# Kernel optimization log

Measured on AMD Instinct MI355X. Metric: run time of the kernel, lower is better.

The kernel has to match this reference:

```python
import jax, jax.numpy as jnp
import numpy as np

N_HEADS = 4
TAU = 0.1

def _ln(x, w, b):
    m = jnp.mean(x, axis=-1, keepdims=True)
    v = jnp.mean(jnp.square(x - m), axis=-1, keepdims=True)
    return (x - m) / jnp.sqrt(v + 1e-6) * w + b

def _l2norm(x):
    # torch F.normalize(dim=1): x / max(||x||_2, 1e-12)
    n = jnp.linalg.norm(x, axis=1, keepdims=True)
    return x / jnp.maximum(n, 1e-12)

def _sincos_pe(T, dim):
    pos = jnp.arange(T, dtype=jnp.float32)[:, None]
    div = jnp.exp(jnp.arange(0, dim, 2, dtype=jnp.float32) * (-np.log(10000.0) / dim))
    ang = pos * div[None, :]
    # interleave: even indices sin, odd indices cos
    return jnp.stack([jnp.sin(ang), jnp.cos(ang)], axis=-1).reshape(T, dim)

def reference(x, p1_w, p1_b, pln1_w, pln1_b, p2_w, pln2_w, pln2_b,
              in_proj_w, in_proj_b, out_proj_w, out_proj_b,
              ln1_w, ln1_b, lin1_w, lin1_b, lin2_w, lin2_b, ln2_w, ln2_b, head_w):
    B, T, D = x.shape
    E = p2_w.shape[0]           # bottleneck_dim = 256
    H = N_HEADS
    hd = E // H
    # projector: Linear -> LN -> GELU -> Linear(no bias) -> LN
    h = jax.nn.gelu(_ln(x.reshape(B * T, D) @ p1_w.T + p1_b, pln1_w, pln1_b), approximate=False)
    h = _ln(h @ p2_w.T, pln2_w, pln2_b).reshape(B, T, E)
    h = h + _sincos_pe(T, E)[None]
    causal = jnp.tril(jnp.ones((T, T), dtype=bool))
    L = in_proj_w.shape[0]
    for i in range(L):  # post-norm TransformerEncoderLayer
        qkv = h @ in_proj_w[i].T + in_proj_b[i]        # [B,T,3E]
        q, k, v = jnp.split(qkv, 3, axis=-1)
        q = q.reshape(B, T, H, hd).transpose(0, 2, 1, 3)
        k = k.reshape(B, T, H, hd).transpose(0, 2, 1, 3)
        v = v.reshape(B, T, H, hd).transpose(0, 2, 1, 3)
        scores = jnp.einsum('bhtd,bhsd->bhts', q, k) / np.float32(np.sqrt(hd))
        scores = jnp.where(causal[None, None], scores, -jnp.inf)
        probs = jax.nn.softmax(scores, axis=-1)        # materialized attn probs (eager path)
        attn = jnp.einsum('bhts,bhsd->bhtd', probs, v).transpose(0, 2, 1, 3).reshape(B, T, E)
        attn = attn @ out_proj_w[i].T + out_proj_b[i]
        h = _ln(h + attn, ln1_w[i], ln1_b[i])
        ff = jax.nn.gelu(h @ lin1_w[i].T + lin1_b[i], approximate=False) @ lin2_w[i].T + lin2_b[i]
        h = _ln(h + ff, ln2_w[i], ln2_b[i])
    flat = _l2norm(h.reshape(B * T, E))
    wn = _l2norm(head_w)
    return (flat @ wn.T / TAU).reshape(B, T, -1)

def setup_inputs() -> dict:
    key = jax.random.key(0)
    ks = jax.random.split(key, 8)
    B, T, D, E, HID, CLS, L = 2048, 20, 2048, 256, 1024, 1000, 2
    s = 0.02
    def w(k, shape):
        return jax.random.normal(k, shape, jnp.float32) * s
    return {
        'x': jax.random.normal(ks[0], (B, T, D), jnp.float32),
        'p1_w': w(ks[1], (HID, D)), 'p1_b': jnp.zeros((HID,), jnp.float32),
        'pln1_w': jnp.ones((HID,), jnp.float32), 'pln1_b': jnp.zeros((HID,), jnp.float32),
        'p2_w': w(ks[2], (E, HID)),
        'pln2_w': jnp.ones((E,), jnp.float32), 'pln2_b': jnp.zeros((E,), jnp.float32),
        'in_proj_w': w(ks[3], (L, 3 * E, E)), 'in_proj_b': jnp.zeros((L, 3 * E), jnp.float32),
        'out_proj_w': w(ks[4], (L, E, E)), 'out_proj_b': jnp.zeros((L, E), jnp.float32),
        'ln1_w': jnp.ones((L, E), jnp.float32), 'ln1_b': jnp.zeros((L, E), jnp.float32),
        'lin1_w': w(ks[5], (L, 4 * E, E)), 'lin1_b': jnp.zeros((L, 4 * E), jnp.float32),
        'lin2_w': w(ks[6], (L, E, 4 * E)), 'lin2_b': jnp.zeros((L, E), jnp.float32),
        'ln2_w': jnp.ones((L, E), jnp.float32), 'ln2_b': jnp.zeros((L, E), jnp.float32),
        'head_w': w(ks[7], (CLS, E)),
    }
```

## Files before the change

kernel.cpp:

```cpp
#include <hip/hip_runtime.h>
#include <math.h>

#define CDIV(a,b) (((a)+(b)-1)/(b))

typedef unsigned short bfu;
typedef short   s16x8 __attribute__((ext_vector_type(8)));
typedef float   f32x4 __attribute__((ext_vector_type(4)));

#define GLOAD16(gp, lp) __builtin_amdgcn_global_load_lds( \
    (const __attribute__((address_space(1))) void*)(gp),  \
    (__attribute__((address_space(3))) void*)(lp), 16, 0, 0)

static __device__ __forceinline__ float gelu_exact(float x) {
    return 0.5f * x * (1.0f + erff(x * 0.7071067811865475f));
}
static __device__ __forceinline__ bfu f2bf(float x) {
    unsigned int u = __float_as_uint(x);
    unsigned int r = u + 0x7fffu + ((u >> 16) & 1u);
    return (bfu)(r >> 16);
}
static __device__ __forceinline__ float bf2f(bfu b) {
    return __uint_as_float(((unsigned int)b) << 16);
}
static __device__ __forceinline__ float wave_sum(float v) {
    #pragma unroll
    for (int off = 32; off; off >>= 1) v += __shfl_xor(v, off, 64);
    return v;
}

__global__ __launch_bounds__(256)
void cvt_kernel(const float* __restrict__ in, bfu* __restrict__ out, int n4)
{
    int i = blockIdx.x * 256 + threadIdx.x;
    const int stride = gridDim.x * 256;
    for (; i < n4; i += stride) {
        float4 f = ((const float4*)in)[i];
        ushort4 o;
        o.x = f2bf(f.x); o.y = f2bf(f.y); o.z = f2bf(f.z); o.w = f2bf(f.w);
        ((ushort4*)out)[i] = o;
    }
}

__global__ __launch_bounds__(256)
void cvt6_kernel(const float* __restrict__ s0, const float* __restrict__ s1,
                 const float* __restrict__ s2, const float* __restrict__ s3,
                 const float* __restrict__ s4, const float* __restrict__ s5,
                 bfu* __restrict__ dst)
{
    const int c0 = 524288;
    const int c1 = c0 + 65536;
    const int c2 = c1 + 98304;
    const int c3 = c2 + 32768;
    const int c4 = c3 + 131072;
    const int c5 = c4 + 131072;
    int i = blockIdx.x * 256 + threadIdx.x;
    const int stride = gridDim.x * 256;
    for (; i < c5; i += stride) {
        const float* s; int base;
        if      (i < c0) { s = s0; base = 0;  }
        else if (i < c1) { s = s1; base = c0; }
        else if (i < c2) { s = s2; base = c1; }
        else if (i < c3) { s = s3; base = c2; }
        else if (i < c4) { s = s4; base = c3; }
        else             { s = s5; base = c4; }
        float4 f = ((const float4*)s)[i - base];
        ushort4 o;
        o.x = f2bf(f.x); o.y = f2bf(f.y); o.z = f2bf(f.z); o.w = f2bf(f.w);
        ((ushort4*)dst)[i] = o;
    }
}

__global__ __launch_bounds__(256)
void pe_kernel(float* __restrict__ pe)
{
    const int t = blockIdx.x;
    const int c = threadIdx.x;
    const float div = expf((float)(c & ~1) * (-9.210340371976184f / 256.0f));
    const float ang = (float)t * div;
    pe[t * 256 + c] = (c & 1) ? cosf(ang) : sinf(ang);
}

template<bool GELU_EP, bool OUT_BF16>
__global__ __launch_bounds__(512, 2)
void mfma_gemm256(const bfu* __restrict__ A, const bfu* __restrict__ W,
                  const float* __restrict__ bias, void* __restrict__ Cv,
                  int M, int N, int K, float scale, int ntx)
{
    __shared__ bfu lds[2][2][8192];

    const int tid  = threadIdx.x;
    const int lane = tid & 63;
    const int wv   = tid >> 6;
    const int nwg  = gridDim.x;
    const int lid  = (nwg & 7) ? (int)blockIdx.x
                               : ((int)blockIdx.x & 7) * (nwg >> 3) + ((int)blockIdx.x >> 3);
    const int row0 = (lid / ntx) * 256;
    const int col0 = (lid % ntx) * 256;

    const int srow = wv * 16 + (lane >> 2);
    const int sk   = ((lane & 3) ^ ((lane >> 2) & 3)) * 8;
    const bfu* aS0 = A + (size_t)(row0 + srow)       * K + sk;
    const bfu* aS1 = A + (size_t)(row0 + srow + 128) * K + sk;
    const bfu* wS0 = W + (size_t)(col0 + srow)       * K + sk;
    const bfu* wS1 = W + (size_t)(col0 + srow + 128) * K + sk;
    const int dOff = wv * 512;

    const int wr = wv >> 2, wc = wv & 3;
    const int fr = lane & 15;
    const int slot = (((lane >> 4) ^ (fr & 3))) * 8;

    f32x4 acc[8][4];
    #pragma unroll
    for (int i = 0; i < 8; ++i)
        #pragma unroll
        for (int j = 0; j < 4; ++j) acc[i][j] = (f32x4)0.f;

    const int nt = K >> 5;

#define STAGE256(b_, t_) do { \
    const size_t ko_ = (size_t)(t_) * 32; \
    GLOAD16(aS0 + ko_, &lds[b_][0][dOff]); \
    GLOAD16(aS1 + ko_, &lds[b_][0][4096 + dOff]); \
    GLOAD16(wS0 + ko_, &lds[b_][1][dOff]); \
    GLOAD16(wS1 + ko_, &lds[b_][1][4096 + dOff]); \
} while (0)

    STAGE256(0, 0);
    STAGE256(1, 1);

    int cur = 0;
    for (int t = 0; t < nt; ++t) {
        if (t + 1 < nt) asm volatile("s_waitcnt vmcnt(4)" ::: "memory");
        else            asm volatile("s_waitcnt vmcnt(0)" ::: "memory");
        asm volatile("s_barrier" ::: "memory");

        const bfu* Ab = lds[cur][0];
        const bfu* Wb = lds[cur][1];

        s16x8 bfr[4], afr[8];
        #pragma unroll
        for (int j = 0; j < 4; ++j)
            bfr[j] = *(const s16x8*)&Wb[(wc * 64 + j * 16 + fr) * 32 + slot];
        #pragma unroll
        for (int i = 0; i < 4; ++i)
            afr[i] = *(const s16x8*)&Ab[(wr * 128 + i * 16 + fr) * 32 + slot];

        __builtin_amdgcn_s_setprio(1);
        #pragma unroll
        for (int i = 0; i < 4; ++i)
            #pragma unroll
            for (int j = 0; j < 4; ++j)
                acc[i][j] = __builtin_amdgcn_mfma_f32_16x16x32_bf16(afr[i], bfr[j], acc[i][j], 0, 0, 0);
        __builtin_amdgcn_s_setprio(0);

        #pragma unroll
        for (int i = 4; i < 8; ++i)
            afr[i] = *(const s16x8*)&Ab[(wr * 128 + i * 16 + fr) * 32 + slot];

        __builtin_amdgcn_s_setprio(1);
        #pragma unroll
        for (int i = 4; i < 8; ++i)
            #pragma unroll
            for (int j = 0; j < 4; ++j)
                acc[i][j] = __builtin_amdgcn_mfma_f32_16x16x32_bf16(afr[i], bfr[j], acc[i][j], 0, 0, 0);
        __builtin_amdgcn_s_setprio(0);

        asm volatile("s_barrier" ::: "memory");
        if (t + 2 < nt) STAGE256(cur, t + 2);
        cur ^= 1;
    }
#undef STAGE256

    #pragma unroll
    for (int i = 0; i < 8; ++i) {
        const int r = row0 + wr * 128 + 16 * i + (lane >> 4) * 4;
        #pragma unroll
        for (int j = 0; j < 4; ++j) {
            const int c = col0 + wc * 64 + 16 * j + fr;
            if (c < N) {
                const float bsum = bias ? bias[c] : 0.f;
                #pragma unroll
                for (int rr = 0; rr < 4; ++rr) {
                    float v = acc[i][j][rr] + bsum;
                    if (GELU_EP) v = gelu_exact(v);
                    v *= scale;
                    if (OUT_BF16) ((bfu*)Cv)[(size_t)(r + rr) * N + c] = f2bf(v);
                    else          ((float*)Cv)[(size_t)(r + rr) * N + c] = v;
                }
            }
        }
    }
}

template<bool RES, bool ADD_PE>
__global__ __launch_bounds__(512, 2)
void mfma_gemm_ln(const bfu* __restrict__ A, const bfu* __restrict__ W,
                  const float* __restrict__ bias, const float* __restrict__ R,
                  const float* __restrict__ lnw, const float* __restrict__ lnb,
                  const float* __restrict__ pe, float* __restrict__ Yf,
                  bfu* __restrict__ Yb, int M, int K, int T)
{
    __shared__ bfu ldsA[2][4096];
    __shared__ bfu ldsW[2][8192];

    const int tid  = threadIdx.x;
    const int lane = tid & 63;
    const int wv   = tid >> 6;
    const int nwg  = gridDim.x;
    const int lid  = (nwg & 7) ? (int)blockIdx.x
                               : ((int)blockIdx.x & 7) * (nwg >> 3) + ((int)blockIdx.x >> 3);
    const int row0 = lid * 128;

    const int srow = wv * 16 + (lane >> 2);
    const int sk   = ((lane & 3) ^ ((lane >> 2) & 3)) * 8;
    const bfu* aS  = A + (size_t)(row0 + srow) * K + sk;
    const bfu* wS0 = W + (size_t)(srow)        * K + sk;
    const bfu* wS1 = W + (size_t)(srow + 128)  * K + sk;
    const int dOff = wv * 512;

    const int wr = wv >> 2, wc = wv & 3;
    const int fr = lane & 15;
    const int g4 = lane >> 4;
    const int slot = ((g4 ^ (fr & 3))) * 8;

    f32x4 acc[4][4];
    #pragma unroll
    for (int i = 0; i < 4; ++i)
        #pragma unroll
        for (int j = 0; j < 4; ++j) acc[i][j] = (f32x4)0.f;

    const int nt = K >> 5;

#define STAGELN(b_, t_) do { \
    const size_t ko_ = (size_t)(t_) * 32; \
    GLOAD16(aS  + ko_, &ldsA[b_][dOff]); \
    GLOAD16(wS0 + ko_, &ldsW[b_][dOff]); \
    GLOAD16(wS1 + ko_, &ldsW[b_][4096 + dOff]); \
} while (0)

    STAGELN(0, 0);
    STAGELN(1, 1);

    int cur = 0;
    for (int t = 0; t < nt; ++t) {
        if (t + 1 < nt) asm volatile("s_waitcnt vmcnt(3)" ::: "memory");
        else            asm volatile("s_waitcnt vmcnt(0)" ::: "memory");
        asm volatile("s_barrier" ::: "memory");

        const bfu* Ab = ldsA[cur];
        const bfu* Wb = ldsW[cur];

        s16x8 bfr[4], afr[4];
        #pragma unroll
        for (int j = 0; j < 4; ++j)
            bfr[j] = *(const s16x8*)&Wb[(wc * 64 + j * 16 + fr) * 32 + slot];
        #pragma unroll
        for (int i = 0; i < 4; ++i)
            afr[i] = *(const s16x8*)&Ab[(wr * 64 + i * 16 + fr) * 32 + slot];

        __builtin_amdgcn_s_setprio(1);
        #pragma unroll
        for (int i = 0; i < 4; ++i)
            #pragma unroll
            for (int j = 0; j < 4; ++j)
                acc[i][j] = __builtin_amdgcn_mfma_f32_16x16x32_bf16(afr[i], bfr[j], acc[i][j], 0, 0, 0);
        __builtin_amdgcn_s_setprio(0);

        asm volatile("s_barrier" ::: "memory");
        if (t + 2 < nt) STAGELN(cur, t + 2);
        cur ^= 1;
    }
#undef STAGELN

    float* red   = (float*)ldsA;
    float* stats = red + 1024;

    float bj[4];
    #pragma unroll
    for (int j = 0; j < 4; ++j)
        bj[j] = bias ? bias[wc * 64 + j * 16 + fr] : 0.f;

    #pragma unroll
    for (int i = 0; i < 4; ++i) {
        #pragma unroll
        for (int rr = 0; rr < 4; ++rr) {
            const int rl = wr * 64 + i * 16 + g4 * 4 + rr;
            const size_t r = (size_t)(row0 + rl);
            float s = 0.f, q = 0.f;
            #pragma unroll
            for (int j = 0; j < 4; ++j) {
                float v = acc[i][j][rr] + bj[j];
                if (RES) v += R[r * 256 + (wc * 64 + j * 16 + fr)];
                acc[i][j][rr] = v;
                s += v; q += v * v;
            }
            #pragma unroll
            for (int off = 1; off < 16; off <<= 1) {
                s += __shfl_xor(s, off, 64);
                q += __shfl_xor(q, off, 64);
            }
            if (fr == 0) { red[rl * 4 + wc] = s; red[512 + rl * 4 + wc] = q; }
        }
    }
    __syncthreads();
    if (tid < 128) {
        const float s = red[tid*4+0] + red[tid*4+1] + red[tid*4+2] + red[tid*4+3];
        const float q = red[512+tid*4+0] + red[512+tid*4+1] + red[512+tid*4+2] + red[512+tid*4+3];
        const float mean = s * (1.f / 256.f);
        const float var  = q * (1.f / 256.f) - mean * mean;
        stats[tid]       = mean;
        stats[128 + tid] = rsqrtf(var + 1e-6f);
    }
    __syncthreads();

    float lw[4], lb[4];
    #pragma unroll
    for (int j = 0; j < 4; ++j) {
        const int c = wc * 64 + j * 16 + fr;
        lw[j] = lnw[c]; lb[j] = lnb[c];
    }
    #pragma unroll
    for (int i = 0; i < 4; ++i) {
        #pragma unroll
        for (int rr = 0; rr < 4; ++rr) {
            const int rl = wr * 64 + i * 16 + g4 * 4 + rr;
            const size_t r = (size_t)(row0 + rl);
            const float mean = stats[rl], rstd = stats[128 + rl];
            const int tmod = (int)(r % (size_t)T);
            #pragma unroll
            for (int j = 0; j < 4; ++j) {
                const int c = wc * 64 + j * 16 + fr;
                float y = (acc[i][j][rr] - mean) * rstd * lw[j] + lb[j];
                if (ADD_PE) y += pe[tmod * 256 + c];
                Yf[r * 256 + c] = y;
                Yb[r * 256 + c] = f2bf(y);
            }
        }
    }
}

__global__ __launch_bounds__(256)
void ln1024_kernel(const bfu* __restrict__ X, const float* __restrict__ w,
                   const float* __restrict__ b, bfu* __restrict__ Y)
{
    __shared__ float sbuf[4];
    const int row = blockIdx.x;
    const bfu* xr = X + (size_t)row * 1024;

    ushort4 t4 = *(const ushort4*)(xr + threadIdx.x * 4);
    float v[4] = {bf2f(t4.x), bf2f(t4.y), bf2f(t4.z), bf2f(t4.w)};

    float s = v[0] + v[1] + v[2] + v[3];
    s = wave_sum(s);
    const int lane = threadIdx.x & 63, wid = threadIdx.x >> 6;
    if (lane == 0) sbuf[wid] = s;
    __syncthreads();
    const float mean = (sbuf[0] + sbuf[1] + sbuf[2] + sbuf[3]) * (1.f / 1024.f);

    float q = 0.f;
    #pragma unroll
    for (int j = 0; j < 4; ++j) { float d = v[j] - mean; q += d * d; }
    q = wave_sum(q);
    __syncthreads();
    if (lane == 0) sbuf[wid] = q;
    __syncthreads();
    const float var  = (sbuf[0] + sbuf[1] + sbuf[2] + sbuf[3]) * (1.f / 1024.f);
    const float rstd = rsqrtf(var + 1e-6f);

    ushort4 o;
    #pragma unroll
    for (int j = 0; j < 4; ++j) {
        const int c = threadIdx.x * 4 + j;
        float y = gelu_exact((v[j] - mean) * rstd * w[c] + b[c]);
        ((bfu*)&o)[j] = f2bf(y);
    }
    *(ushort4*)(Y + (size_t)row * 1024 + threadIdx.x * 4) = o;
}

__global__ __launch_bounds__(64)
void attn_kernel(const bfu* __restrict__ qkv, bfu* __restrict__ out,
                 int B, int T, int H)
{
    __shared__ float qs[20][65];
    __shared__ float ks[20][65];
    __shared__ float vs[20][65];
    __shared__ float probs[64];

    const int blk = blockIdx.x;
    const int b = blk / H;
    const int h = blk % H;
    const int tid = threadIdx.x;

    for (int t = 0; t < T; ++t) {
        const bfu* base = qkv + (size_t)(b * T + t) * 768 + h * 64 + tid;
        qs[t][tid] = bf2f(base[0]);
        ks[t][tid] = bf2f(base[256]);
        vs[t][tid] = bf2f(base[512]);
    }
    __syncthreads();

    for (int t = 0; t < T; ++t) {
        float sc = -INFINITY;
        if (tid <= t) {
            float s = 0.f;
            #pragma unroll
            for (int d = 0; d < 64; ++d) s = fmaf(qs[t][d], ks[tid][d], s);
            sc = s * 0.125f;
        }
        float m = sc;
        #pragma unroll
        for (int off = 32; off; off >>= 1) m = fmaxf(m, __shfl_xor(m, off, 64));
        float p = (tid <= t) ? expf(sc - m) : 0.f;
        float sum = p;
        #pragma unroll
        for (int off = 32; off; off >>= 1) sum += __shfl_xor(sum, off, 64);
        p /= sum;
        probs[tid] = p;
        __syncthreads();

        float o = 0.f;
        for (int s = 0; s <= t; ++s) o = fmaf(probs[s], vs[s][tid], o);
        out[(size_t)(b * T + t) * 256 + h * 64 + tid] = f2bf(o);
        __syncthreads();
    }
}

__global__ __launch_bounds__(256)
void l2norm_kernel(const float* __restrict__ X, bfu* __restrict__ Y)
{
    const int row  = blockIdx.x * 4 + (threadIdx.x >> 6);
    const int lane = threadIdx.x & 63;
    float4 v = *(const float4*)(X + (size_t)row * 256 + lane * 4);
    float n = sqrtf(wave_sum(v.x*v.x + v.y*v.y + v.z*v.z + v.w*v.w));
    n = 1.f / fmaxf(n, 1e-12f);
    ushort4 o = {f2bf(v.x*n), f2bf(v.y*n), f2bf(v.z*n), f2bf(v.w*n)};
    *(ushort4*)(Y + (size_t)row * 256 + lane * 4) = o;
}

extern "C" void kernel_launch(void* const* d_in, const int* in_sizes, int n_in,
                              void* d_out, int out_size, void* d_ws, size_t ws_size,
                              hipStream_t stream)
{
    const float* x         = (const float*)d_in[0];
    const float* p1_w      = (const float*)d_in[1];
    const float* p1_b      = (const float*)d_in[2];
    const float* pln1_w    = (const float*)d_in[3];
    const float* pln1_b    = (const float*)d_in[4];
    const float* p2_w      = (const float*)d_in[5];
    const float* pln2_w    = (const float*)d_in[6];
    const float* pln2_b    = (const float*)d_in[7];
    const float* in_proj_w = (const float*)d_in[8];
    const float* in_proj_b = (const float*)d_in[9];
    const float* out_proj_w= (const float*)d_in[10];
    const float* out_proj_b= (const float*)d_in[11];
    const float* ln1_w     = (const float*)d_in[12];
    const float* ln1_b     = (const float*)d_in[13];
    const float* lin1_w    = (const float*)d_in[14];
    const float* lin1_b    = (const float*)d_in[15];
    const float* lin2_w    = (const float*)d_in[16];
    const float* lin2_b    = (const float*)d_in[17];
    const float* ln2_w     = (const float*)d_in[18];
    const float* ln2_b     = (const float*)d_in[19];
    const float* head_w    = (const float*)d_in[20];

    const int B = 2048, T = 20, E = 256, HID = 1024, CLS = 1000, L = 2, H = 4;
    const int M = B * T;
    const int D = 2048;

    char* p = (char*)d_ws;
    bfu*   xb     = (bfu*)p;    p += (size_t)M * D * 2;
    bfu*   h1b    = (bfu*)p;    p += (size_t)M * HID * 2;
    bfu*   wblk   = (bfu*)p;    p += (size_t)3932160 * 2;
    bfu*   wnb    = (bfu*)p;    p += (size_t)1024 * E * 2;
    float* pe     = (float*)p;  p += (size_t)T * 256 * 4;

    char* q = (char*)xb;
    float* h      = (float*)q;  q += (size_t)M * E * 4;
    bfu*   hb     = (bfu*)q;    q += (size_t)M * E * 2;
    bfu*   abf    = (bfu*)q;    q += (size_t)M * E * 2;

    bfu* p1wb  = wblk;
    bfu* p2wb  = p1wb  + (size_t)HID * D;
    bfu* qkvwb = p2wb  + (size_t)E * HID;
    bfu* outwb = qkvwb + (size_t)L * 3 * E * E;
    bfu* l1wb  = outwb + (size_t)L * E * E;
    bfu* l2wb  = l1wb  + (size_t)L * 4 * E * E;

    float* out   = (float*)d_out;
    bfu*   qkvb  = (bfu*)d_out;

    cvt_kernel<<<2048, 256, 0, stream>>>(x, xb, M * D / 4);
    cvt6_kernel<<<2048, 256, 0, stream>>>(p1_w, p2_w, in_proj_w, out_proj_w, lin1_w, lin2_w, wblk);
    pe_kernel<<<T, 256, 0, stream>>>(pe);

    mfma_gemm256<false, true><<<dim3((M/256) * (HID/256)), 512, 0, stream>>>(
        xb, p1wb, p1_b, h1b, M, HID, D, 1.f, HID/256);
    ln1024_kernel<<<M, 256, 0, stream>>>(h1b, pln1_w, pln1_b, h1b);
    mfma_gemm_ln<false, true><<<dim3(M/128), 512, 0, stream>>>(
        h1b, p2wb, nullptr, nullptr, pln2_w, pln2_b, pe, h, hb, M, HID, T);

    for (int l = 0; l < L; ++l) {
        mfma_gemm256<false, true><<<dim3(3 * (M/256)), 512, 0, stream>>>(
            hb, qkvwb + (size_t)l * 3*E*E, in_proj_b + (size_t)l * 3*E, qkvb, M, 3*E, E, 1.f, 3);
        attn_kernel<<<B * H, 64, 0, stream>>>(qkvb, abf, B, T, H);
        mfma_gemm_ln<true, false><<<dim3(M/128), 512, 0, stream>>>(
            abf, outwb + (size_t)l * E*E, out_proj_b + (size_t)l * E, h,
            ln1_w + (size_t)l * E, ln1_b + (size_t)l * E, nullptr, h, hb, M, E, T);
        mfma_gemm256<true, true><<<dim3(4 * (M/256)), 512, 0, stream>>>(
            hb, l1wb + (size_t)l * 4*E*E, lin1_b + (size_t)l * 4*E, h1b, M, HID, E, 1.f, 4);
        mfma_gemm_ln<true, false><<<dim3(M/128), 512, 0, stream>>>(
            h1b, l2wb + (size_t)l * E*4*E, lin2_b + (size_t)l * E, h,
            ln2_w + (size_t)l * E, ln2_b + (size_t)l * E, nullptr, h, hb, M, HID, T);
    }

    l2norm_kernel<<<M/4, 256, 0, stream>>>(h, hb);
    l2norm_kernel<<<CLS/4, 256, 0, stream>>>(head_w, wnb);
    mfma_gemm256<false, false><<<dim3(4 * (M/256)), 512, 0, stream>>>(
        hb, wnb, nullptr, out, M, CLS, E, 10.f, 4);
}
```

Measured before the change: 1.234 ms.

## Fuse final L2 normalization into last GEMM+LN, refine LDS swizzle, vectorize attention loads

The last layer's FFN-output GEMM+LayerNorm kernel now also computes each row's L2 norm with a cross-wave reduction in shared memory. It writes the normalized bf16 rows directly, which removes the separate l2norm kernel launch and the fp32 write and re-read of h. The LDS swizzle in both MFMA GEMM kernels adds an extra XOR term to cut bank conflicts on fragment reads. The attention kernel loads Q, K and V with 8-byte vector loads instead of scalar 2-byte loads. The new swizzle must stay consistent between the staging writes and the fragment reads, or results will be wrong.

```diff
diff --git a/kernel.cpp b/kernel.cpp
--- a/kernel.cpp
+++ b/kernel.cpp
@@ -98,7 +98,7 @@
     const int col0 = (lid % ntx) * 256;
 
     const int srow = wv * 16 + (lane >> 2);
-    const int sk   = ((lane & 3) ^ ((lane >> 2) & 3)) * 8;
+    const int sk   = ((lane & 3) ^ ((lane >> 2) & 3) ^ (lane >> 4)) * 8;
     const bfu* aS0 = A + (size_t)(row0 + srow)       * K + sk;
     const bfu* aS1 = A + (size_t)(row0 + srow + 128) * K + sk;
     const bfu* wS0 = W + (size_t)(col0 + srow)       * K + sk;
@@ -107,7 +107,7 @@
 
     const int wr = wv >> 2, wc = wv & 3;
     const int fr = lane & 15;
-    const int slot = (((lane >> 4) ^ (fr & 3))) * 8;
+    const int slot = (((lane >> 4) ^ (fr & 3) ^ ((fr >> 2) & 3))) * 8;
 
     f32x4 acc[8][4];
     #pragma unroll
@@ -192,7 +192,7 @@
     }
 }
 
-template<bool RES, bool ADD_PE>
+template<bool RES, bool ADD_PE, bool L2N>
 __global__ __launch_bounds__(512, 2)
 void mfma_gemm_ln(const bfu* __restrict__ A, const bfu* __restrict__ W,
                   const float* __restrict__ bias, const float* __restrict__ R,
@@ -212,7 +212,7 @@
     const int row0 = lid * 128;
 
     const int srow = wv * 16 + (lane >> 2);
-    const int sk   = ((lane & 3) ^ ((lane >> 2) & 3)) * 8;
+    const int sk   = ((lane & 3) ^ ((lane >> 2) & 3) ^ (lane >> 4)) * 8;
     const bfu* aS  = A + (size_t)(row0 + srow) * K + sk;
     const bfu* wS0 = W + (size_t)(srow)        * K + sk;
     const bfu* wS1 = W + (size_t)(srow + 128)  * K + sk;
@@ -221,7 +221,7 @@
     const int wr = wv >> 2, wc = wv & 3;
     const int fr = lane & 15;
     const int g4 = lane >> 4;
-    const int slot = ((g4 ^ (fr & 3))) * 8;
+    const int slot = ((g4 ^ (fr & 3) ^ ((fr >> 2) & 3))) * 8;
 
     f32x4 acc[4][4];
     #pragma unroll
@@ -327,13 +327,46 @@
             const size_t r = (size_t)(row0 + rl);
             const float mean = stats[rl], rstd = stats[128 + rl];
             const int tmod = (int)(r % (size_t)T);
+            float ysq = 0.f;
             #pragma unroll
             for (int j = 0; j < 4; ++j) {
                 const int c = wc * 64 + j * 16 + fr;
                 float y = (acc[i][j][rr] - mean) * rstd * lw[j] + lb[j];
                 if (ADD_PE) y += pe[tmod * 256 + c];
-                Yf[r * 256 + c] = y;
-                Yb[r * 256 + c] = f2bf(y);
+                if (!L2N) {
+                    Yf[r * 256 + c] = y;
+                    Yb[r * 256 + c] = f2bf(y);
+                } else {
+                    acc[i][j][rr] = y;
+                    ysq += y * y;
+                }
+            }
+            if (L2N) {
+                #pragma unroll
+                for (int off = 1; off < 16; off <<= 1) ysq += __shfl_xor(ysq, off, 64);
+                if (fr == 0) red[rl * 4 + wc] = ysq;
+            }
+        }
+    }
+    if (L2N) {
+        __syncthreads();
+        if (tid < 128) {
+            const float n = sqrtf(red[tid*4+0] + red[tid*4+1] + red[tid*4+2] + red[tid*4+3]);
+            stats[tid] = 1.f / fmaxf(n, 1e-12f);
+        }
+        __syncthreads();
+        #pragma unroll
+        for (int i = 0; i < 4; ++i) {
+            #pragma unroll
+            for (int rr = 0; rr < 4; ++rr) {
+                const int rl = wr * 64 + i * 16 + g4 * 4 + rr;
+                const size_t r = (size_t)(row0 + rl);
+                const float rn = stats[rl];
+                #pragma unroll
+                for (int j = 0; j < 4; ++j) {
+                    const int c = wc * 64 + j * 16 + fr;
+                    Yb[r * 256 + c] = f2bf(acc[i][j][rr] * rn);
+                }
             }
         }
     }
@@ -391,11 +424,19 @@
     const int h = blk % H;
     const int tid = threadIdx.x;
 
-    for (int t = 0; t < T; ++t) {
-        const bfu* base = qkv + (size_t)(b * T + t) * 768 + h * 64 + tid;
-        qs[t][tid] = bf2f(base[0]);
-        ks[t][tid] = bf2f(base[256]);
-        vs[t][tid] = bf2f(base[512]);
+    const bfu* base0 = qkv + (size_t)(b * T) * 768 + h * 64;
+    #pragma unroll
+    for (int m = 0; m < 3; ++m) {
+        const bfu* src = base0 + m * 256;
+        float (*dst)[65] = (m == 0) ? qs : (m == 1) ? ks : vs;
+        #pragma unroll
+        for (int i = 0; i < 5; ++i) {
+            const int idx = i * 64 + tid;
+            const int t = idx >> 4, s = (idx & 15) * 4;
+            ushort4 u = *(const ushort4*)(src + (size_t)t * 768 + s);
+            dst[t][s+0] = bf2f(u.x); dst[t][s+1] = bf2f(u.y);
+            dst[t][s+2] = bf2f(u.z); dst[t][s+3] = bf2f(u.w);
+        }
     }
     __syncthreads();
 
@@ -496,24 +537,29 @@
     mfma_gemm256<false, true><<<dim3((M/256) * (HID/256)), 512, 0, stream>>>(
         xb, p1wb, p1_b, h1b, M, HID, D, 1.f, HID/256);
     ln1024_kernel<<<M, 256, 0, stream>>>(h1b, pln1_w, pln1_b, h1b);
-    mfma_gemm_ln<false, true><<<dim3(M/128), 512, 0, stream>>>(
+    mfma_gemm_ln<false, true, false><<<dim3(M/128), 512, 0, stream>>>(
         h1b, p2wb, nullptr, nullptr, pln2_w, pln2_b, pe, h, hb, M, HID, T);
 
     for (int l = 0; l < L; ++l) {
         mfma_gemm256<false, true><<<dim3(3 * (M/256)), 512, 0, stream>>>(
             hb, qkvwb + (size_t)l * 3*E*E, in_proj_b + (size_t)l * 3*E, qkvb, M, 3*E, E, 1.f, 3);
         attn_kernel<<<B * H, 64, 0, stream>>>(qkvb, abf, B, T, H);
-        mfma_gemm_ln<true, false><<<dim3(M/128), 512, 0, stream>>>(
+        mfma_gemm_ln<true, false, false><<<dim3(M/128), 512, 0, stream>>>(
             abf, outwb + (size_t)l * E*E, out_proj_b + (size_t)l * E, h,
             ln1_w + (size_t)l * E, ln1_b + (size_t)l * E, nullptr, h, hb, M, E, T);
         mfma_gemm256<true, true><<<dim3(4 * (M/256)), 512, 0, stream>>>(
             hb, l1wb + (size_t)l * 4*E*E, lin1_b + (size_t)l * 4*E, h1b, M, HID, E, 1.f, 4);
-        mfma_gemm_ln<true, false><<<dim3(M/128), 512, 0, stream>>>(
-            h1b, l2wb + (size_t)l * E*4*E, lin2_b + (size_t)l * E, h,
-            ln2_w + (size_t)l * E, ln2_b + (size_t)l * E, nullptr, h, hb, M, HID, T);
-    }
-
-    l2norm_kernel<<<M/4, 256, 0, stream>>>(h, hb);
+        if (l < L - 1) {
+            mfma_gemm_ln<true, false, false><<<dim3(M/128), 512, 0, stream>>>(
+                h1b, l2wb + (size_t)l * E*4*E, lin2_b + (size_t)l * E, h,
+                ln2_w + (size_t)l * E, ln2_b + (size_t)l * E, nullptr, h, hb, M, HID, T);
+        } else {
+            mfma_gemm_ln<true, false, true><<<dim3(M/128), 512, 0, stream>>>(
+                h1b, l2wb + (size_t)l * E*4*E, lin2_b + (size_t)l * E, h,
+                ln2_w + (size_t)l * E, ln2_b + (size_t)l * E, nullptr, nullptr, hb, M, HID, T);
+        }
+    }
+
     l2norm_kernel<<<CLS/4, 256, 0, stream>>>(head_w, wnb);
     mfma_gemm256<false, false><<<dim3(4 * (M/256)), 512, 0, stream>>>(
         hb, wnb, nullptr, out, M, CLS, E, 10.f, 4);
```

New measurement: 1.258 ms. Within noise of the previous version (+2.0%).
